# Kernel tuning notes

Measured on AMD Instinct MI355X. Metric: run time of the kernel, lower is better.

Reference implementation:

```python
import jax, jax.numpy as jnp
import numpy as np

B, T, IN, H, OUT = 2048, 512, 6, 32, 64


def setup_inputs() -> dict:
    key = jax.random.key(0)
    ks = jax.random.split(key, 13)
    s_in = 1.0 / np.sqrt(H)  # torch LSTM/Linear default uniform bound
    u = lambda k, shape, s: jax.random.uniform(k, shape, jnp.float32, -s, s)
    return {
        "imu": jax.random.normal(ks[0], (B, T, IN), jnp.float32),
        # layer 0 (input_size=6)
        "w_ih0": u(ks[1], (4 * H, IN), s_in),
        "w_hh0": u(ks[2], (4 * H, H), s_in),
        "b_ih0": u(ks[3], (4 * H,), s_in),
        "b_hh0": u(ks[4], (4 * H,), s_in),
        # layer 1 (input_size=32)
        "w_ih1": u(ks[5], (4 * H, H), s_in),
        "w_hh1": u(ks[6], (4 * H, H), s_in),
        "b_ih1": u(ks[7], (4 * H,), s_in),
        "b_hh1": u(ks[8], (4 * H,), s_in),
        # heads
        "wf": u(ks[9], (OUT, H), s_in),
        "bf": u(ks[10], (OUT,), s_in),
        "wn": u(ks[11], (OUT, H), s_in),
        "bn": u(ks[12], (OUT,), s_in),
    }


def _lstm_layer(x, w_ih, w_hh, b_ih, b_hh):
    # x: [B, T, in] -> h sequence [B, T, H]; torch gate order: i, f, g, o
    b = x.shape[0]
    # precompute input contribution once: [B, T, 4H]
    gx = jnp.einsum("bti,gi->btg", x, w_ih) + b_ih + b_hh

    def step(carry, g_t):
        h, c = carry
        gates = g_t + h @ w_hh.T  # [B, 4H]
        i = jax.nn.sigmoid(gates[:, :H])
        f = jax.nn.sigmoid(gates[:, H:2 * H])
        g = jnp.tanh(gates[:, 2 * H:3 * H])
        o = jax.nn.sigmoid(gates[:, 3 * H:])
        c = f * c + i * g
        h = o * jnp.tanh(c)
        return (h, c), h

    h0 = jnp.zeros((b, H), x.dtype)
    (_, _), hs = jax.lax.scan(step, (h0, h0), jnp.swapaxes(gx, 0, 1))
    return jnp.swapaxes(hs, 0, 1)  # [B, T, H]


def reference(imu, w_ih0, w_hh0, b_ih0, b_hh0, w_ih1, w_hh1, b_ih1, b_hh1, wf, bf, wn, bn):
    h = _lstm_layer(imu, w_ih0, w_hh0, b_ih0, b_hh0)
    h = _lstm_layer(h, w_ih1, w_hh1, b_ih1, b_hh1)
    last = h[:, -1, :]  # [B, H]
    a_i = last @ wf.T + bf
    R_i = jnp.exp(last @ wn.T + bn)
    return (a_i, R_i)
```

## Files before the change

kernel.cpp:

```cpp
#include <hip/hip_runtime.h>
#include <hip/hip_bf16.h>

#define TT 512
#define BPB 16
#define NBLK (2048 / BPB)
#define OUTD 64

typedef __attribute__((ext_vector_type(8))) short short8;
typedef __attribute__((ext_vector_type(4))) float f32x4;

__device__ __forceinline__ short f2bf(float x) {
    union { float f; unsigned u; } v; v.f = x;
    unsigned r = (v.u + 0x7FFFu + ((v.u >> 16) & 1u)) >> 16;
    return (short)r;
}
__device__ __forceinline__ short cvt_bf16(float x) {
    unsigned r;
    asm("v_cvt_pk_bf16_f32 %0, %1, %1" : "=v"(r) : "v"(x));
    return (short)r;
}
__device__ __forceinline__ float sigm(float x) {
    return __builtin_amdgcn_rcpf(1.f + __expf(-x));
}
__device__ __forceinline__ float tanh_fast(float x) {
    return 2.f * sigm(2.f * x) - 1.f;
}

#define ACT_UPDATE(acc, c, hval)                                   \
    {                                                              \
        float gi = sigm((acc)[0]);                                 \
        float gf = sigm((acc)[1]);                                 \
        float gg = tanh_fast((acc)[2]);                            \
        float go = sigm((acc)[3]);                                 \
        (c) = gf * (c) + gi * gg;                                  \
        (hval) = go * tanh_fast((c));                              \
    }

__global__ __launch_bounds__(1024, 1) void lstm2_dense_kernel(
    const float* __restrict__ imu,
    const float* __restrict__ w_ih0, const float* __restrict__ w_hh0,
    const float* __restrict__ b_ih0, const float* __restrict__ b_hh0,
    const float* __restrict__ w_ih1, const float* __restrict__ w_hh1,
    const float* __restrict__ b_ih1, const float* __restrict__ b_hh1,
    const float* __restrict__ wf, const float* __restrict__ bf,
    const float* __restrict__ wn, const float* __restrict__ bn,
    float* __restrict__ out)
{
    const int tid   = threadIdx.x;
    const int l     = tid & 63;
    const int w     = tid >> 6;
    const int layer = w >> 3;
    const int tau   = w & 7;
    const int c     = l & 15;
    const int q     = l >> 4;
    const int unit  = 4 * tau + q;

    __shared__ __align__(16) short xfrag[TT + 4][BPB][8];
    __shared__ __align__(16) short h1f[2][16][40];
    __shared__ __align__(16) short h2f[2][16][40];
    __shared__ __align__(16) float lasth[16][36];

    {
        short* p1 = &h1f[0][0][0];
        short* p2 = &h2f[0][0][0];
        for (int i = tid; i < 2 * 16 * 40; i += 1024) { p1[i] = 0; p2[i] = 0; }
        short* px = &xfrag[TT][0][0];
        if (tid < 4 * BPB * 8) px[tid] = 0;
    }

    {
        const int bg0 = blockIdx.x * BPB;
        for (int p = tid; p < BPB * TT; p += 1024) {
            const int bb = p >> 9;
            const int t  = p & (TT - 1);
            const float* src = imu + ((size_t)(bg0 + bb) * TT + t) * 6;
            float2 a0 = *(const float2*)(src);
            float2 a1 = *(const float2*)(src + 2);
            float2 a2 = *(const float2*)(src + 4);
            unsigned* dst = (unsigned*)&xfrag[t][bb][0];
            dst[0] = (unsigned short)f2bf(a0.x) | ((unsigned)(unsigned short)f2bf(a0.y) << 16);
            dst[1] = (unsigned short)f2bf(a1.x) | ((unsigned)(unsigned short)f2bf(a1.y) << 16);
            dst[2] = (unsigned short)f2bf(a2.x) | ((unsigned)(unsigned short)f2bf(a2.y) << 16);
            dst[3] = 0u;
        }
    }

    const int G = (c & 3) * 32 + 4 * tau + (c >> 2);
    short8 AF, AS;
    f32x4 bias;
    if (layer == 0) {
        #pragma unroll
        for (int j = 0; j < 8; ++j) {
            AF[j] = (q == 0 && j < 6) ? f2bf(w_ih0[G * 6 + j]) : (short)0;
            AS[j] = f2bf(w_hh0[G * 32 + q * 8 + j]);
        }
        #pragma unroll
        for (int r = 0; r < 4; ++r)
            bias[r] = b_ih0[r * 32 + unit] + b_hh0[r * 32 + unit];
    } else {
        #pragma unroll
        for (int j = 0; j < 8; ++j) {
            AF[j] = f2bf(w_ih1[G * 32 + q * 8 + j]);
            AS[j] = f2bf(w_hh1[G * 32 + q * 8 + j]);
        }
        #pragma unroll
        for (int r = 0; r < 4; ++r)
            bias[r] = b_ih1[r * 32 + unit] + b_hh1[r * 32 + unit];
    }

    float cst = 0.f;

    const short8* h1r0 = (const short8*)&h1f[0][c][q * 8];
    const short8* h1r1 = (const short8*)&h1f[1][c][q * 8];
    const short8* h2r0 = (const short8*)&h2f[0][c][q * 8];
    const short8* h2r1 = (const short8*)&h2f[1][c][q * 8];

    __syncthreads();

    short8 xvE = (short8)0, xvO = (short8)0;
    f32x4 xacc = bias;
    if (layer == 0) {
        short8 xv = *(const short8*)&xfrag[0][c][0];
        f32x4 a = __builtin_amdgcn_mfma_f32_16x16x32_bf16(AF, xv, bias, 0, 0, 0);
        float h;
        ACT_UPDATE(a, cst, h);
        h1f[1][c][unit] = cvt_bf16(h);
        short8 xv1 = *(const short8*)&xfrag[1][c][0];
        xacc = __builtin_amdgcn_mfma_f32_16x16x32_bf16(AF, xv1, bias, 0, 0, 0);
        xvE = *(const short8*)&xfrag[2][c][0];
    }
    __syncthreads();

#define STEP(T, H1R, H2R, WP, XVC, XVL)                                         \
    {                                                                           \
        if (layer == 0) {                                                       \
            short8 hv = *(H1R);                                                 \
            f32x4 a = __builtin_amdgcn_mfma_f32_16x16x32_bf16(AS, hv, xacc, 0, 0, 0); \
            float h;                                                            \
            ACT_UPDATE(a, cst, h);                                              \
            h1f[WP][c][unit] = cvt_bf16(h);                                     \
            xacc = __builtin_amdgcn_mfma_f32_16x16x32_bf16(AF, XVC, bias, 0, 0, 0); \
            XVL = *(const short8*)&xfrag[(T) + 3][c][0];                        \
        } else {                                                                \
            short8 av = *(H1R);                                                 \
            short8 bv = *(H2R);                                                 \
            f32x4 a = __builtin_amdgcn_mfma_f32_16x16x32_bf16(AF, av, bias, 0, 0, 0); \
            a = __builtin_amdgcn_mfma_f32_16x16x32_bf16(AS, bv, a, 0, 0, 0);    \
            float h;                                                            \
            ACT_UPDATE(a, cst, h);                                              \
            h2f[WP][c][unit] = cvt_bf16(h);                                     \
        }                                                                       \
        __syncthreads();                                                        \
    }

    #pragma unroll 1
    for (int t = 0; t < TT - 2; t += 2) {
        STEP(t,     h1r1, h2r1, 0, xvE, xvO)
        STEP(t + 1, h1r0, h2r0, 1, xvO, xvE)
    }
    STEP(TT - 2, h1r1, h2r1, 0, xvE, xvO)

    if (layer == 1) {
        short8 av = *h1r0;
        short8 bv = *h2r0;
        f32x4 a = __builtin_amdgcn_mfma_f32_16x16x32_bf16(AF, av, bias, 0, 0, 0);
        a = __builtin_amdgcn_mfma_f32_16x16x32_bf16(AS, bv, a, 0, 0, 0);
        float h;
        ACT_UPDATE(a, cst, h);
        lasth[c][unit] = h;
    }
    __syncthreads();

    {
        const int bb = tid >> 6;
        const int o  = tid & 63;
        float accF = bf[o], accN = bn[o];
        const float4* wf4 = (const float4*)(wf + o * 32);
        const float4* wn4 = (const float4*)(wn + o * 32);
        const float4* hv4 = (const float4*)&lasth[bb][0];
        #pragma unroll
        for (int k = 0; k < 8; ++k) {
            float4 h4 = hv4[k];
            float4 f4 = wf4[k];
            float4 n4 = wn4[k];
            accF += f4.x * h4.x + f4.y * h4.y + f4.z * h4.z + f4.w * h4.w;
            accN += n4.x * h4.x + n4.y * h4.y + n4.z * h4.z + n4.w * h4.w;
        }
        const size_t bg = (size_t)blockIdx.x * BPB + bb;
        out[bg * OUTD + o] = accF;
        out[(size_t)2048 * OUTD + bg * OUTD + o] = __expf(accN);
    }
}

extern "C" void kernel_launch(void* const* d_in, const int* in_sizes, int n_in,
                              void* d_out, int out_size, void* d_ws, size_t ws_size,
                              hipStream_t stream) {
    const float* imu   = (const float*)d_in[0];
    const float* w_ih0 = (const float*)d_in[1];
    const float* w_hh0 = (const float*)d_in[2];
    const float* b_ih0 = (const float*)d_in[3];
    const float* b_hh0 = (const float*)d_in[4];
    const float* w_ih1 = (const float*)d_in[5];
    const float* w_hh1 = (const float*)d_in[6];
    const float* b_ih1 = (const float*)d_in[7];
    const float* b_hh1 = (const float*)d_in[8];
    const float* wf    = (const float*)d_in[9];
    const float* bf    = (const float*)d_in[10];
    const float* wn    = (const float*)d_in[11];
    const float* bn    = (const float*)d_in[12];
    float* out = (float*)d_out;

    lstm2_dense_kernel<<<dim3(NBLK), dim3(1024), 0, stream>>>(
        imu, w_ih0, w_hh0, b_ih0, b_hh0,
        w_ih1, w_hh1, b_ih1, b_hh1,
        wf, bf, wn, bn, out);
}
```

Before: 209.6 us.

## Restructure LSTM into two-wave blocks with shuffle-based hidden-state exchange

Each block now handles 2 batch rows with 2 waves, one per layer, instead of 16 rows spread over 16 waves. Each wave computes all 8 gate tiles itself and keeps only its own tile, accepting redundant MFMA work. The layer's hidden state is repacked into the MFMA fragment with cross-lane shuffles rather than a round trip through shared memory. The aim is to spread the work over more CUs, cut the cost of the 16-wave barrier down to a 2-wave one, and remove shared-memory hops from the serial recurrence. In exchange each step carries about 8x more MFMAs plus shuffle overhead on the dependent chain, and register pressure rises from keeping 8 weight tiles per lane.

```diff
diff --git a/kernel.cpp b/kernel.cpp
--- a/kernel.cpp
+++ b/kernel.cpp
@@ -2,22 +2,23 @@
 #include <hip/hip_bf16.h>
 
 #define TT 512
-#define BPB 16
+#define BPB 2
 #define NBLK (2048 / BPB)
 #define OUTD 64
 
 typedef __attribute__((ext_vector_type(8))) short short8;
 typedef __attribute__((ext_vector_type(4))) float f32x4;
+typedef __attribute__((ext_vector_type(4))) unsigned uint4v;
 
 __device__ __forceinline__ short f2bf(float x) {
     union { float f; unsigned u; } v; v.f = x;
     unsigned r = (v.u + 0x7FFFu + ((v.u >> 16) & 1u)) >> 16;
     return (short)r;
 }
-__device__ __forceinline__ short cvt_bf16(float x) {
+__device__ __forceinline__ unsigned cvtpk2(float lo, float hi) {
     unsigned r;
-    asm("v_cvt_pk_bf16_f32 %0, %1, %1" : "=v"(r) : "v"(x));
-    return (short)r;
+    asm("v_cvt_pk_bf16_f32 %0, %1, %2" : "=v"(r) : "v"(lo), "v"(hi));
+    return r;
 }
 __device__ __forceinline__ float sigm(float x) {
     return __builtin_amdgcn_rcpf(1.f + __expf(-x));
@@ -36,7 +37,36 @@
         (hval) = go * tanh_fast((c));                              \
     }
 
-__global__ __launch_bounds__(1024, 1) void lstm2_dense_kernel(
+#define MFMA __builtin_amdgcn_mfma_f32_16x16x32_bf16
+
+#define SELECT(mine, acc)                                          \
+    f32x4 mine;                                                    \
+    {                                                              \
+        f32x4 m01 = (tsel & 1) ? (acc)[1] : (acc)[0];              \
+        f32x4 m23 = (tsel & 1) ? (acc)[3] : (acc)[2];              \
+        f32x4 m45 = (tsel & 1) ? (acc)[5] : (acc)[4];              \
+        f32x4 m67 = (tsel & 1) ? (acc)[7] : (acc)[6];              \
+        f32x4 mA  = (tsel & 2) ? m23 : m01;                        \
+        f32x4 mB  = (tsel & 2) ? m67 : m45;                        \
+        mine = (tsel & 4) ? mB : mA;                               \
+    }
+
+#define REPACK(h, d0, d1, d2, d3)                                  \
+    {                                                              \
+        const int base = 4 * kg + b;                               \
+        float s0 = __shfl((h), base);                              \
+        float s1 = __shfl((h), base + 16);                         \
+        float s2 = __shfl((h), base + 32);                         \
+        float s3 = __shfl((h), base + 48);                         \
+        float s4 = __shfl((h), base + 2);                          \
+        float s5 = __shfl((h), base + 18);                         \
+        float s6 = __shfl((h), base + 34);                         \
+        float s7 = __shfl((h), base + 50);                         \
+        d0 = cvtpk2(s0, s1); d1 = cvtpk2(s2, s3);                  \
+        d2 = cvtpk2(s4, s5); d3 = cvtpk2(s6, s7);                  \
+    }
+
+__global__ __launch_bounds__(128, 2) void lstm2_pairwave_kernel(
     const float* __restrict__ imu,
     const float* __restrict__ w_ih0, const float* __restrict__ w_hh0,
     const float* __restrict__ b_ih0, const float* __restrict__ b_hh0,
@@ -46,31 +76,22 @@
     const float* __restrict__ wn, const float* __restrict__ bn,
     float* __restrict__ out)
 {
-    const int tid   = threadIdx.x;
-    const int l     = tid & 63;
-    const int w     = tid >> 6;
-    const int layer = w >> 3;
-    const int tau   = w & 7;
-    const int c     = l & 15;
-    const int q     = l >> 4;
-    const int unit  = 4 * tau + q;
-
-    __shared__ __align__(16) short xfrag[TT + 4][BPB][8];
-    __shared__ __align__(16) short h1f[2][16][40];
-    __shared__ __align__(16) short h2f[2][16][40];
-    __shared__ __align__(16) float lasth[16][36];
-
-    {
-        short* p1 = &h1f[0][0][0];
-        short* p2 = &h2f[0][0][0];
-        for (int i = tid; i < 2 * 16 * 40; i += 1024) { p1[i] = 0; p2[i] = 0; }
-        short* px = &xfrag[TT][0][0];
-        if (tid < 4 * BPB * 8) px[tid] = 0;
-    }
+    const int tid  = threadIdx.x;
+    const int l    = tid & 63;
+    const int wv   = tid >> 6;
+    const int col  = l & 15;
+    const int kg   = l >> 4;
+    const int b    = col & 1;
+    const int tsel = col >> 1;
+    const int unit = 4 * tsel + kg;
+
+    __shared__ __align__(16) short    xfrag[TT + 2][BPB][8];
+    __shared__ __align__(16) unsigned h1buf[2][BPB][4][4];
+    __shared__ __align__(16) float    lasth[BPB][36];
 
     {
         const int bg0 = blockIdx.x * BPB;
-        for (int p = tid; p < BPB * TT; p += 1024) {
+        for (int p = tid; p < BPB * TT; p += 128) {
             const int bb = p >> 9;
             const int t  = p & (TT - 1);
             const float* src = imu + ((size_t)(bg0 + bb) * TT + t) * 6;
@@ -83,91 +104,116 @@
             dst[2] = (unsigned short)f2bf(a2.x) | ((unsigned)(unsigned short)f2bf(a2.y) << 16);
             dst[3] = 0u;
         }
-    }
-
-    const int G = (c & 3) * 32 + 4 * tau + (c >> 2);
-    short8 AF, AS;
-    f32x4 bias;
-    if (layer == 0) {
-        #pragma unroll
-        for (int j = 0; j < 8; ++j) {
-            AF[j] = (q == 0 && j < 6) ? f2bf(w_ih0[G * 6 + j]) : (short)0;
-            AS[j] = f2bf(w_hh0[G * 32 + q * 8 + j]);
+        short* px = &xfrag[TT][0][0];
+        if (tid < 2 * BPB * 8) px[tid] = 0;
+    }
+
+    const int m = col;
+    short8 AS[8], AX[8];
+    f32x4 bias[8];
+    #pragma unroll
+    for (int tp = 0; tp < 8; ++tp) {
+        const int G = (m & 3) * 32 + 4 * tp + (m >> 2);
+        const int u = 4 * tp + kg;
+        if (wv == 0) {
+            #pragma unroll
+            for (int j = 0; j < 8; ++j) {
+                AX[tp][j] = (kg == 0 && j < 6) ? f2bf(w_ih0[G * 6 + j]) : (short)0;
+                AS[tp][j] = f2bf(w_hh0[G * 32 + kg * 8 + j]);
+            }
+            #pragma unroll
+            for (int r = 0; r < 4; ++r)
+                bias[tp][r] = b_ih0[r * 32 + u] + b_hh0[r * 32 + u];
+        } else {
+            #pragma unroll
+            for (int j = 0; j < 8; ++j) {
+                AX[tp][j] = f2bf(w_ih1[G * 32 + kg * 8 + j]);
+                AS[tp][j] = f2bf(w_hh1[G * 32 + kg * 8 + j]);
+            }
+            #pragma unroll
+            for (int r = 0; r < 4; ++r)
+                bias[tp][r] = b_ih1[r * 32 + u] + b_hh1[r * 32 + u];
         }
-        #pragma unroll
-        for (int r = 0; r < 4; ++r)
-            bias[r] = b_ih0[r * 32 + unit] + b_hh0[r * 32 + unit];
-    } else {
-        #pragma unroll
-        for (int j = 0; j < 8; ++j) {
-            AF[j] = f2bf(w_ih1[G * 32 + q * 8 + j]);
-            AS[j] = f2bf(w_hh1[G * 32 + q * 8 + j]);
-        }
-        #pragma unroll
-        for (int r = 0; r < 4; ++r)
-            bias[r] = b_ih1[r * 32 + unit] + b_hh1[r * 32 + unit];
     }
 
     float cst = 0.f;
-
-    const short8* h1r0 = (const short8*)&h1f[0][c][q * 8];
-    const short8* h1r1 = (const short8*)&h1f[1][c][q * 8];
-    const short8* h2r0 = (const short8*)&h2f[0][c][q * 8];
-    const short8* h2r1 = (const short8*)&h2f[1][c][q * 8];
+    short8 hfrag = (short8)0;
+    f32x4 accx[8];
+    short8 xvE = (short8)0, xvO = (short8)0;
 
     __syncthreads();
 
-    short8 xvE = (short8)0, xvO = (short8)0;
-    f32x4 xacc = bias;
-    if (layer == 0) {
-        short8 xv = *(const short8*)&xfrag[0][c][0];
-        f32x4 a = __builtin_amdgcn_mfma_f32_16x16x32_bf16(AF, xv, bias, 0, 0, 0);
-        float h;
-        ACT_UPDATE(a, cst, h);
-        h1f[1][c][unit] = cvt_bf16(h);
-        short8 xv1 = *(const short8*)&xfrag[1][c][0];
-        xacc = __builtin_amdgcn_mfma_f32_16x16x32_bf16(AF, xv1, bias, 0, 0, 0);
-        xvE = *(const short8*)&xfrag[2][c][0];
-    }
-    __syncthreads();
-
-#define STEP(T, H1R, H2R, WP, XVC, XVL)                                         \
+    if (wv == 0) {
+        short8 xv0 = *(const short8*)&xfrag[0][b][0];
+        #pragma unroll
+        for (int tp = 0; tp < 8; ++tp)
+            accx[tp] = MFMA(AX[tp], xv0, bias[tp], 0, 0, 0);
+        xvE = *(const short8*)&xfrag[1][b][0];
+    }
+
+#define STEP(I, RP, WP, XVC, XVL, ACT2)                                         \
     {                                                                           \
-        if (layer == 0) {                                                       \
-            short8 hv = *(H1R);                                                 \
-            f32x4 a = __builtin_amdgcn_mfma_f32_16x16x32_bf16(AS, hv, xacc, 0, 0, 0); \
+        if (wv == 0) {                                                          \
+            f32x4 acc[8];                                                       \
+            _Pragma("unroll")                                                   \
+            for (int tp = 0; tp < 8; ++tp)                                      \
+                acc[tp] = MFMA(AS[tp], hfrag, accx[tp], 0, 0, 0);               \
+            SELECT(mine, acc);                                                  \
             float h;                                                            \
-            ACT_UPDATE(a, cst, h);                                              \
-            h1f[WP][c][unit] = cvt_bf16(h);                                     \
-            xacc = __builtin_amdgcn_mfma_f32_16x16x32_bf16(AF, XVC, bias, 0, 0, 0); \
-            XVL = *(const short8*)&xfrag[(T) + 3][c][0];                        \
-        } else {                                                                \
-            short8 av = *(H1R);                                                 \
-            short8 bv = *(H2R);                                                 \
-            f32x4 a = __builtin_amdgcn_mfma_f32_16x16x32_bf16(AF, av, bias, 0, 0, 0); \
-            a = __builtin_amdgcn_mfma_f32_16x16x32_bf16(AS, bv, a, 0, 0, 0);    \
+            ACT_UPDATE(mine, cst, h);                                           \
+            unsigned d0, d1, d2, d3;                                            \
+            REPACK(h, d0, d1, d2, d3);                                          \
+            union { unsigned u[4]; short8 s; } hu;                              \
+            hu.u[0] = d0; hu.u[1] = d1; hu.u[2] = d2; hu.u[3] = d3;             \
+            hfrag = hu.s;                                                       \
+            if (col < 2)                                                        \
+                *(uint4v*)&h1buf[WP][col][kg][0] = (uint4v){d0, d1, d2, d3};    \
+            _Pragma("unroll")                                                   \
+            for (int tp = 0; tp < 8; ++tp)                                      \
+                accx[tp] = MFMA(AX[tp], XVC, bias[tp], 0, 0, 0);                \
+            XVL = *(const short8*)&xfrag[(I) + 2][b][0];                        \
+        } else if (ACT2) {                                                      \
+            short8 h1v = *(const short8*)&h1buf[RP][b][kg][0];                  \
+            f32x4 acc[8];                                                       \
+            _Pragma("unroll")                                                   \
+            for (int tp = 0; tp < 8; ++tp)                                      \
+                acc[tp] = MFMA(AS[tp], hfrag, bias[tp], 0, 0, 0);               \
+            _Pragma("unroll")                                                   \
+            for (int tp = 0; tp < 8; ++tp)                                      \
+                acc[tp] = MFMA(AX[tp], h1v, acc[tp], 0, 0, 0);                  \
+            SELECT(mine, acc);                                                  \
             float h;                                                            \
-            ACT_UPDATE(a, cst, h);                                              \
-            h2f[WP][c][unit] = cvt_bf16(h);                                     \
+            ACT_UPDATE(mine, cst, h);                                           \
+            unsigned d0, d1, d2, d3;                                            \
+            REPACK(h, d0, d1, d2, d3);                                          \
+            union { unsigned u[4]; short8 s; } hu;                              \
+            hu.u[0] = d0; hu.u[1] = d1; hu.u[2] = d2; hu.u[3] = d3;             \
+            hfrag = hu.s;                                                       \
         }                                                                       \
         __syncthreads();                                                        \
     }
 
+    STEP(0, 0, 0, xvE, xvO, 0)
     #pragma unroll 1
-    for (int t = 0; t < TT - 2; t += 2) {
-        STEP(t,     h1r1, h2r1, 0, xvE, xvO)
-        STEP(t + 1, h1r0, h2r0, 1, xvO, xvE)
-    }
-    STEP(TT - 2, h1r1, h2r1, 0, xvE, xvO)
-
-    if (layer == 1) {
-        short8 av = *h1r0;
-        short8 bv = *h2r0;
-        f32x4 a = __builtin_amdgcn_mfma_f32_16x16x32_bf16(AF, av, bias, 0, 0, 0);
-        a = __builtin_amdgcn_mfma_f32_16x16x32_bf16(AS, bv, a, 0, 0, 0);
+    for (int t = 1; t < TT - 1; t += 2) {
+        STEP(t,     0, 1, xvO, xvE, 1)
+        STEP(t + 1, 1, 0, xvE, xvO, 1)
+    }
+    STEP(TT - 1, 0, 1, xvO, xvE, 1)
+
+    if (wv == 1) {
+        short8 h1v = *(const short8*)&h1buf[1][b][kg][0];
+        f32x4 acc[8];
+        #pragma unroll
+        for (int tp = 0; tp < 8; ++tp)
+            acc[tp] = MFMA(AS[tp], hfrag, bias[tp], 0, 0, 0);
+        #pragma unroll
+        for (int tp = 0; tp < 8; ++tp)
+            acc[tp] = MFMA(AX[tp], h1v, acc[tp], 0, 0, 0);
+        SELECT(mine, acc);
         float h;
-        ACT_UPDATE(a, cst, h);
-        lasth[c][unit] = h;
+        ACT_UPDATE(mine, cst, h);
+        lasth[b][unit] = h;
     }
     __syncthreads();
 
@@ -210,7 +256,7 @@
     const float* bn    = (const float*)d_in[12];
     float* out = (float*)d_out;
 
-    lstm2_dense_kernel<<<dim3(NBLK), dim3(1024), 0, stream>>>(
+    lstm2_pairwave_kernel<<<dim3(NBLK), dim3(128), 0, stream>>>(
         imu, w_ih0, w_hh0, b_ih0, b_hh0,
         w_ih1, w_hh1, b_ih1, b_hh1,
         wf, bf, wn, bn, out);
```

Result: slower. 284.2 us (+35.6%).
